# Performance work log

Measured on AMD Instinct MI355X. Metric: run time of the kernel, lower is better.

Reference implementation:

```python
import jax, jax.numpy as jnp
import numpy as np

B, N, D, H, DK = 4, 2048, 1024, 16, 64  # batch, seq, model_dim, heads, key_dim (= value_dim)
NEG = -1e9


def setup_inputs() -> dict:
    key = jax.random.key(0)
    ks = jax.random.split(key, 5)
    X = jax.random.normal(ks[0], (B, N, D), dtype=jnp.float32)
    # causal additive mask [N, N]; module slices mask[:N, :M] and adds to logits
    mask = jnp.where(jnp.tril(jnp.ones((N, N), dtype=bool)), 0.0, NEG).astype(jnp.float32)
    s = 1.0 / np.sqrt(D)
    Wq = jax.random.normal(ks[1], (D, H * DK), dtype=jnp.float32) * s
    Wk = jax.random.normal(ks[2], (D, H * DK), dtype=jnp.float32) * s
    Wv = jax.random.normal(ks[3], (D, H * DK), dtype=jnp.float32) * s
    Wo = jax.random.normal(ks[4], (H * DK, D), dtype=jnp.float32) * s
    return {"X": X, "mask": mask, "Wq": Wq, "Wk": Wk, "Wv": Wv, "Wo": Wo}


def reference(X, mask, Wq, Wk, Wv, Wo):
    # Linear projections (bias=False), then split heads: [B,N,H,DK] -> [B,H,N,DK]
    Q = (X @ Wq).reshape(B, N, H, DK).transpose(0, 2, 1, 3)
    K = (X @ Wk).reshape(B, N, H, DK).transpose(0, 2, 1, 3)
    V = (X @ Wv).reshape(B, N, H, DK).transpose(0, 2, 1, 3)
    # full [B,H,N,N] attention logits (module materializes it explicitly)
    att = jnp.einsum('bhnd,bhmd->bhnm', Q, K) / jnp.sqrt(jnp.float32(DK))
    # dropout is in eval mode here -> identity; then additive mask[:N,:M]
    att = att + mask[:N, :N]
    prob = jax.nn.softmax(att, axis=-1)
    values = jnp.einsum('bhnm,bhmd->bhnd', prob, V)
    values_cat = values.transpose(0, 2, 1, 3).reshape(B, N, H * DK)
    return values_cat @ Wo
```

## Files before the change

kernel.cpp:

```cpp
#include <hip/hip_runtime.h>

typedef __fp16   f2  __attribute__((ext_vector_type(2)));
typedef _Float16 h4  __attribute__((ext_vector_type(4)));
typedef _Float16 v8h __attribute__((ext_vector_type(8)));
typedef float    v4f __attribute__((ext_vector_type(4)));
struct f2x2 { f2 lo, hi; };

constexpr int Bn = 4, Nn = 2048, Dn = 1024, Hn = 16, DKn = 64, Mn = 8192;

__device__ __forceinline__ void load_lds16(const _Float16* g, _Float16* l) {
    __builtin_amdgcn_global_load_lds(
        (const __attribute__((address_space(1))) void*)g,
        (__attribute__((address_space(3))) void*)l, 16, 0, 0);
}

__global__ __launch_bounds__(256) void cast_f16(const float* __restrict__ x,
                                                _Float16* __restrict__ y) {
    const int i = blockIdx.x * 256 + threadIdx.x;
    const float4 v = ((const float4*)x)[i];
    h4 o; o[0] = (_Float16)v.x; o[1] = (_Float16)v.y;
    o[2] = (_Float16)v.z; o[3] = (_Float16)v.w;
    ((h4*)y)[i] = o;
}

__global__ __launch_bounds__(256) void castW4(const float* __restrict__ Wq,
                                              const float* __restrict__ Wk,
                                              const float* __restrict__ Wv,
                                              const float* __restrict__ Wo,
                                              _Float16* __restrict__ Wqkv,
                                              _Float16* __restrict__ Wto) {
    __shared__ float tile[32][33];
    const int which = blockIdx.x >> 10, bid = blockIdx.x & 1023;
    const float* W = which == 0 ? Wq : which == 1 ? Wk : which == 2 ? Wv : Wo;
    _Float16* Dst = which < 3 ? (Wqkv + ((size_t)which << 20)) : Wto;
    const int bx = bid & 31, by = bid >> 5;
    const int t = threadIdx.x;
    const int r = t >> 3, c4 = (t & 7) * 4;
    const float4 v = *(const float4*)&W[(size_t)(by * 32 + r) * Dn + bx * 32 + c4];
    tile[r][c4 + 0] = v.x; tile[r][c4 + 1] = v.y;
    tile[r][c4 + 2] = v.z; tile[r][c4 + 3] = v.w;
    __syncthreads();
    h4 o;
    o[0] = (_Float16)tile[c4 + 0][r];
    o[1] = (_Float16)tile[c4 + 1][r];
    o[2] = (_Float16)tile[c4 + 2][r];
    o[3] = (_Float16)tile[c4 + 3][r];
    *(h4*)&Dst[(size_t)(bx * 32 + r) * Dn + by * 32 + c4] = o;
}

#define GEMM_KLOOP64(Abase, Bbase)                                                  \
    v4f acc[4][4];                                                                  \
    _Pragma("unroll") for (int i = 0; i < 4; ++i)                                   \
        _Pragma("unroll") for (int j = 0; j < 4; ++j) acc[i][j] = v4f{0,0,0,0};     \
    for (int k0 = 0; k0 < Dn; k0 += 64) {                                           \
        __syncthreads();                                                            \
        _Pragma("unroll") for (int jj = 0; jj < 4; ++jj) {                          \
            const int ci = jj * 256 + w * 64 + lane;                                \
            const int rs = ci >> 3, cs = ci & 7;                                    \
            const int gc = (cs ^ (rs & 7)) * 8;                                     \
            load_lds16(Abase + (size_t)rs * Dn + k0 + gc, &As[(jj*256 + w*64) * 8]);\
            load_lds16(Bbase + (size_t)rs * Dn + k0 + gc, &Bs[(jj*256 + w*64) * 8]);\
        }                                                                           \
        __syncthreads();                                                            \
        _Pragma("unroll") for (int ks2 = 0; ks2 < 2; ++ks2) {                       \
            v8h a[4], b[4];                                                         \
            _Pragma("unroll") for (int i = 0; i < 4; ++i) {                         \
                const int ar = wm*64 + i*16 + l16;                                  \
                a[i] = *(const v8h*)&As[ar * 64 + (((ks2*4 + quad) ^ (ar & 7)) * 8)];\
            }                                                                       \
            _Pragma("unroll") for (int j = 0; j < 4; ++j) {                         \
                const int br = wn*64 + j*16 + l16;                                  \
                b[j] = *(const v8h*)&Bs[br * 64 + (((ks2*4 + quad) ^ (br & 7)) * 8)];\
            }                                                                       \
            _Pragma("unroll") for (int i = 0; i < 4; ++i)                           \
                _Pragma("unroll") for (int j = 0; j < 4; ++j)                       \
                    acc[i][j] = __builtin_amdgcn_mfma_f32_16x16x32_f16(a[i], b[j],  \
                                                                   acc[i][j],0,0,0);\
        }                                                                           \
    }

__global__ __launch_bounds__(256) void gemmqkv(const _Float16* __restrict__ A,
                                               const _Float16* __restrict__ Wt,
                                               _Float16* __restrict__ Qo,
                                               _Float16* __restrict__ Ko,
                                               _Float16* __restrict__ Vo)
{
    __shared__ __align__(16) _Float16 As[128 * 64];
    __shared__ __align__(16) _Float16 Bs[128 * 64];
    const int t = threadIdx.x, lane = t & 63, w = t >> 6;
    const int quad = lane >> 4, l16 = lane & 15;
    const int wm = w >> 1, wn = w & 1;
    const int bx = blockIdx.x % 24, by = blockIdx.x / 24;
    const int m0 = by * 128, n0 = bx * 128;
    const _Float16* Abase = A + (size_t)m0 * Dn;
    const _Float16* Bbase = Wt + (size_t)n0 * Dn;

    GEMM_KLOOP64(Abase, Bbase)

    const int sec = n0 >> 10;
    if (sec < 2) {
        _Float16* C = sec ? Ko : Qo;
        const float scale = sec ? 1.0f : 0.125f * 1.44269504f;
#pragma unroll
        for (int i = 0; i < 4; ++i) {
            const int mbase = m0 + wm * 64 + i * 16 + quad * 4;
#pragma unroll
            for (int j = 0; j < 4; ++j) {
                const int nl = (n0 + wn * 64 + j * 16 + l16) & 1023;
                const int h = nl >> 6, dk = nl & 63;
#pragma unroll
                for (int r = 0; r < 4; ++r) {
                    const int m = mbase + r, b = m >> 11, nr = m & (Nn - 1);
                    C[((size_t)(b * Hn + h) * Nn + nr) * DKn + dk] = (_Float16)(acc[i][j][r] * scale);
                }
            }
        }
    } else {
#pragma unroll
        for (int i = 0; i < 4; ++i) {
            const int mbase = m0 + wm * 64 + i * 16 + quad * 4;
            const int b = mbase >> 11, nr = mbase & (Nn - 1);
#pragma unroll
            for (int j = 0; j < 4; ++j) {
                const int nl = (n0 + wn * 64 + j * 16 + l16) & 1023;
                const int h = nl >> 6, dk = nl & 63;
                h4 o; o[0] = (_Float16)acc[i][j][0]; o[1] = (_Float16)acc[i][j][1];
                o[2] = (_Float16)acc[i][j][2]; o[3] = (_Float16)acc[i][j][3];
                *(h4*)&Vo[((size_t)(b * Hn + h) * DKn + dk) * Nn + nr] = o;
            }
        }
    }
}

__global__ __launch_bounds__(256) void gemmo(const _Float16* __restrict__ A,
                                             const _Float16* __restrict__ Wt,
                                             float* __restrict__ C)
{
    __shared__ __align__(16) _Float16 As[128 * 64];
    __shared__ __align__(16) _Float16 Bs[128 * 64];
    const int t = threadIdx.x, lane = t & 63, w = t >> 6;
    const int quad = lane >> 4, l16 = lane & 15;
    const int wm = w >> 1, wn = w & 1;
    const int bx = blockIdx.x & 7, by = blockIdx.x >> 3;
    const int m0 = by * 128, n0 = bx * 128;
    const _Float16* Abase = A + (size_t)m0 * Dn;
    const _Float16* Bbase = Wt + (size_t)n0 * Dn;

    GEMM_KLOOP64(Abase, Bbase)

#pragma unroll
    for (int i = 0; i < 4; ++i) {
        const int mbase = m0 + wm * 64 + i * 16 + quad * 4;
#pragma unroll
        for (int j = 0; j < 4; ++j) {
            const int n = n0 + wn * 64 + j * 16 + l16;
#pragma unroll
            for (int r = 0; r < 4; ++r)
                C[(size_t)(mbase + r) * Dn + n] = acc[i][j][r];
        }
    }
}

__global__ __launch_bounds__(256) void flashv5(const _Float16* __restrict__ Q,
                                               const _Float16* __restrict__ K,
                                               const _Float16* __restrict__ Vt,
                                               _Float16* __restrict__ O)
{
    __shared__ __align__(16) _Float16 KS[64 * 64];
    __shared__ __align__(16) _Float16 VS[64 * 64];
    __shared__ __align__(16) _Float16 Ps[4][32 * 64];

    const int t = threadIdx.x;
    const int lane = t & 63, w = t >> 6;
    const int quad = lane >> 4, l16 = lane & 15;
    const int bh = blockIdx.x & 63;
    const int qtile = 15 - (blockIdx.x >> 6);
    const int b = bh >> 4, h = bh & 15;
    const int qb = qtile * 128 + w * 32;

    const _Float16* Qg = Q  + (size_t)bh * Nn * DKn;
    const _Float16* Kg = K  + (size_t)bh * Nn * DKn;
    const _Float16* Vg = Vt + (size_t)bh * DKn * Nn;

    auto stage = [&](int kt) {
        const int k0 = kt * 64;
#pragma unroll
        for (int jj = 0; jj < 2; ++jj) {
            const int ci = jj * 256 + w * 64 + lane;
            const int r = ci >> 3, c = ci & 7;
            const int gc = (c ^ (r & 7)) * 8;
            load_lds16(Kg + (size_t)(k0 + r) * DKn + gc, &KS[(jj * 256 + w * 64) * 8]);
            load_lds16(Vg + (size_t)r * Nn + k0 + gc,    &VS[(jj * 256 + w * 64) * 8]);
        }
    };
#define SWZ(arr, r, c) (*(const v8h*)&(arr)[(r) * 64 + (((c) ^ ((r) & 7)) * 8)])

    v8h qf[2][2];
#pragma unroll
    for (int qq = 0; qq < 2; ++qq)
#pragma unroll
        for (int ks = 0; ks < 2; ++ks)
            qf[qq][ks] = *(const v8h*)&Qg[(size_t)(qb + qq * 16 + l16) * DKn + ks * 32 + quad * 8];

    v8h ones;
#pragma unroll
    for (int i = 0; i < 8; ++i) ones[i] = (_Float16)1.0f;

    v4f o[2][4];
#pragma unroll
    for (int mq = 0; mq < 2; ++mq)
#pragma unroll
        for (int nt = 0; nt < 4; ++nt) o[mq][nt] = v4f{0.f, 0.f, 0.f, 0.f};
    v4f ol[2] = {v4f{0.f, 0.f, 0.f, 0.f}, v4f{0.f, 0.f, 0.f, 0.f}};

    const int NKT  = 2 * qtile + 2;
    const int diag = 2 * qtile + (w >> 1);

    for (int kt = 0; kt < NKT; ++kt) {
        stage(kt);
        __syncthreads();
        if (kt <= diag) {
            const int k0 = kt * 64;
            auto ptile = [&](bool domask) {
#pragma unroll
                for (int kk = 0; kk < 4; ++kk) {
                    v4f s0 = v4f{0.f, 0.f, 0.f, 0.f}, s1 = v4f{0.f, 0.f, 0.f, 0.f};
#pragma unroll
                    for (int ks = 0; ks < 2; ++ks) {
                        const v8h ak = SWZ(KS, kk * 16 + l16, ks * 4 + quad);
                        s0 = __builtin_amdgcn_mfma_f32_16x16x32_f16(ak, qf[0][ks], s0, 0, 0, 0);
                        s1 = __builtin_amdgcn_mfma_f32_16x16x32_f16(ak, qf[1][ks], s1, 0, 0, 0);
                    }
                    const int key0 = k0 + kk * 16 + quad * 4;
#pragma unroll
                    for (int qq = 0; qq < 2; ++qq) {
                        const v4f sv = qq ? s1 : s0;
                        const int q = qb + qq * 16 + l16;
                        float p[4];
#pragma unroll
                        for (int r = 0; r < 4; ++r) {
                            float x = sv[r];
                            if (domask) x = (key0 + r > q) ? -1e9f : x;
                            p[r] = exp2f(x);
                        }
                        f2x2 pkr;
                        pkr.lo = __builtin_amdgcn_cvt_pkrtz(p[0], p[1]);
                        pkr.hi = __builtin_amdgcn_cvt_pkrtz(p[2], p[3]);
                        const h4 pk = __builtin_bit_cast(h4, pkr);
                        const int prow = qq * 16 + l16;
                        const int pch  = kk * 2 + (quad >> 1);
                        *(h4*)&Ps[w][prow * 64 + ((pch ^ (prow & 7)) * 8 + (quad & 1) * 4)] = pk;
                    }
                }
#pragma unroll
                for (int ks = 0; ks < 2; ++ks)
#pragma unroll
                    for (int mq = 0; mq < 2; ++mq) {
                        const int arow = mq * 16 + l16;
                        const int ach  = ks * 4 + quad;
                        const v8h a = *(const v8h*)&Ps[w][arow * 64 + ((ach ^ (arow & 7)) * 8)];
#pragma unroll
                        for (int nt = 0; nt < 4; ++nt) {
                            const v8h bvv = SWZ(VS, nt * 16 + l16, ks * 4 + quad);
                            o[mq][nt] = __builtin_amdgcn_mfma_f32_16x16x32_f16(a, bvv, o[mq][nt], 0, 0, 0);
                        }
                        ol[mq] = __builtin_amdgcn_mfma_f32_16x16x32_f16(a, ones, ol[mq], 0, 0, 0);
                    }
            };
            if (kt == diag) ptile(true); else ptile(false);
        }
        __syncthreads();
    }
#undef SWZ

    _Float16* Op = O + (size_t)b * Nn * Dn + h * DKn;
#pragma unroll
    for (int mq = 0; mq < 2; ++mq)
#pragma unroll
        for (int r = 0; r < 4; ++r) {
            const float li = 1.0f / ol[mq][r];
            const int qrow = qb + mq * 16 + quad * 4 + r;
#pragma unroll
            for (int nt = 0; nt < 4; ++nt)
                Op[(size_t)qrow * Dn + nt * 16 + l16] = (_Float16)(o[mq][nt][r] * li);
        }
}

extern "C" void kernel_launch(void* const* d_in, const int* in_sizes, int n_in,
                              void* d_out, int out_size, void* d_ws, size_t ws_size,
                              hipStream_t stream)
{
    const float* X  = (const float*)d_in[0];
    const float* Wq = (const float*)d_in[2];
    const float* Wk = (const float*)d_in[3];
    const float* Wv = (const float*)d_in[4];
    const float* Wo = (const float*)d_in[5];

    char* ws = (char*)d_ws;
    _Float16* Xh   = (_Float16*)ws;
    _Float16* Wqkv = (_Float16*)(ws + (16u << 20));
    _Float16* Wto  = Wqkv + (3u << 20);
    _Float16* Qh   = Wto + (1u << 20);
    _Float16* Kh   = Qh + (size_t)Mn * Dn;
    _Float16* Vth  = Kh + (size_t)Mn * Dn;
    _Float16* Ah   = Vth + (size_t)Mn * Dn;

    cast_f16<<<(Mn * Dn / 4) / 256, 256, 0, stream>>>(X, Xh);
    castW4<<<4096, 256, 0, stream>>>(Wq, Wk, Wv, Wo, Wqkv, Wto);
    gemmqkv<<<64 * 24, 256, 0, stream>>>(Xh, Wqkv, Qh, Kh, Vth);
    flashv5<<<1024, 256, 0, stream>>>(Qh, Kh, Vth, Ah);
    gemmo<<<512, 256, 0, stream>>>(Ah, Wto, (float*)d_out);
}
```

Measured before the change: 262.6 us.

## Shrink output GEMM tile to 128x64, precompute LDS offsets, use native exp2

The output projection GEMM now uses 128x64 tiles with its own inline K-loop, doubling the grid to 1024 blocks so more CUs have work. In the flash attention kernel, swizzled LDS offsets for K, V and P are computed once per thread instead of inside the loop, and exp2f is replaced by the hardware exp2 builtin when it is available. The trade-offs are more redundant A-tile loads in the GEMM, extra registers held for the offset tables in attention, and possibly slightly different exp2 accuracy.

```diff
diff --git a/kernel.cpp b/kernel.cpp
--- a/kernel.cpp
+++ b/kernel.cpp
@@ -5,6 +5,12 @@
 typedef _Float16 v8h __attribute__((ext_vector_type(8)));
 typedef float    v4f __attribute__((ext_vector_type(4)));
 struct f2x2 { f2 lo, hi; };
+
+#if __has_builtin(__builtin_amdgcn_exp2f)
+#define FEXP2(x) __builtin_amdgcn_exp2f(x)
+#else
+#define FEXP2(x) exp2f(x)
+#endif
 
 constexpr int Bn = 4, Nn = 2048, Dn = 1024, Hn = 16, DKn = 64, Mn = 8192;
 
@@ -137,23 +143,65 @@
                                              float* __restrict__ C)
 {
     __shared__ __align__(16) _Float16 As[128 * 64];
-    __shared__ __align__(16) _Float16 Bs[128 * 64];
+    __shared__ __align__(16) _Float16 Bs[64 * 64];
     const int t = threadIdx.x, lane = t & 63, w = t >> 6;
     const int quad = lane >> 4, l16 = lane & 15;
     const int wm = w >> 1, wn = w & 1;
-    const int bx = blockIdx.x & 7, by = blockIdx.x >> 3;
-    const int m0 = by * 128, n0 = bx * 128;
+    const int bx = blockIdx.x & 15, by = blockIdx.x >> 4;
+    const int m0 = by * 128, n0 = bx * 64;
     const _Float16* Abase = A + (size_t)m0 * Dn;
     const _Float16* Bbase = Wt + (size_t)n0 * Dn;
 
-    GEMM_KLOOP64(Abase, Bbase)
+    v4f acc[4][2];
+#pragma unroll
+    for (int i = 0; i < 4; ++i)
+#pragma unroll
+        for (int j = 0; j < 2; ++j) acc[i][j] = v4f{0.f, 0.f, 0.f, 0.f};
+
+    for (int k0 = 0; k0 < Dn; k0 += 64) {
+        __syncthreads();
+#pragma unroll
+        for (int jj = 0; jj < 4; ++jj) {
+            const int ci = jj * 256 + w * 64 + lane;
+            const int rs = ci >> 3, cs = ci & 7;
+            const int gc = (cs ^ (rs & 7)) * 8;
+            load_lds16(Abase + (size_t)rs * Dn + k0 + gc, &As[(jj * 256 + w * 64) * 8]);
+        }
+#pragma unroll
+        for (int jj = 0; jj < 2; ++jj) {
+            const int ci = jj * 256 + w * 64 + lane;
+            const int rs = ci >> 3, cs = ci & 7;
+            const int gc = (cs ^ (rs & 7)) * 8;
+            load_lds16(Bbase + (size_t)rs * Dn + k0 + gc, &Bs[(jj * 256 + w * 64) * 8]);
+        }
+        __syncthreads();
+#pragma unroll
+        for (int ks2 = 0; ks2 < 2; ++ks2) {
+            v8h a[4], b[2];
+#pragma unroll
+            for (int i = 0; i < 4; ++i) {
+                const int ar = wm * 64 + i * 16 + l16;
+                a[i] = *(const v8h*)&As[ar * 64 + (((ks2 * 4 + quad) ^ (ar & 7)) * 8)];
+            }
+#pragma unroll
+            for (int j = 0; j < 2; ++j) {
+                const int br = wn * 32 + j * 16 + l16;
+                b[j] = *(const v8h*)&Bs[br * 64 + (((ks2 * 4 + quad) ^ (br & 7)) * 8)];
+            }
+#pragma unroll
+            for (int i = 0; i < 4; ++i)
+#pragma unroll
+                for (int j = 0; j < 2; ++j)
+                    acc[i][j] = __builtin_amdgcn_mfma_f32_16x16x32_f16(a[i], b[j], acc[i][j], 0, 0, 0);
+        }
+    }
 
 #pragma unroll
     for (int i = 0; i < 4; ++i) {
         const int mbase = m0 + wm * 64 + i * 16 + quad * 4;
 #pragma unroll
-        for (int j = 0; j < 4; ++j) {
-            const int n = n0 + wn * 64 + j * 16 + l16;
+        for (int j = 0; j < 2; ++j) {
+            const int n = n0 + wn * 32 + j * 16 + l16;
 #pragma unroll
             for (int r = 0; r < 4; ++r)
                 C[(size_t)(mbase + r) * Dn + n] = acc[i][j][r];
@@ -193,7 +241,6 @@
             load_lds16(Vg + (size_t)r * Nn + k0 + gc,    &VS[(jj * 256 + w * 64) * 8]);
         }
     };
-#define SWZ(arr, r, c) (*(const v8h*)&(arr)[(r) * 64 + (((c) ^ ((r) & 7)) * 8)])
 
     v8h qf[2][2];
 #pragma unroll
@@ -201,6 +248,31 @@
 #pragma unroll
         for (int ks = 0; ks < 2; ++ks)
             qf[qq][ks] = *(const v8h*)&Qg[(size_t)(qb + qq * 16 + l16) * DKn + ks * 32 + quad * 8];
+
+    int koff[4][2], voff[4][2], pwoff[2][4], proff[2][2];
+#pragma unroll
+    for (int kk = 0; kk < 4; ++kk)
+#pragma unroll
+        for (int ks = 0; ks < 2; ++ks) {
+            const int kr = kk * 16 + l16, kc = ks * 4 + quad;
+            koff[kk][ks] = kr * 64 + ((kc ^ (kr & 7)) * 8);
+            const int vr = kk * 16 + l16;
+            voff[kk][ks] = vr * 64 + ((kc ^ (vr & 7)) * 8);
+        }
+#pragma unroll
+    for (int qq = 0; qq < 2; ++qq) {
+        const int prow = qq * 16 + l16;
+#pragma unroll
+        for (int kk = 0; kk < 4; ++kk) {
+            const int pch = kk * 2 + (quad >> 1);
+            pwoff[qq][kk] = prow * 64 + ((pch ^ (prow & 7)) * 8 + (quad & 1) * 4);
+        }
+#pragma unroll
+        for (int ks = 0; ks < 2; ++ks) {
+            const int ach = ks * 4 + quad;
+            proff[qq][ks] = prow * 64 + ((ach ^ (prow & 7)) * 8);
+        }
+    }
 
     v8h ones;
 #pragma unroll
@@ -227,7 +299,7 @@
                     v4f s0 = v4f{0.f, 0.f, 0.f, 0.f}, s1 = v4f{0.f, 0.f, 0.f, 0.f};
 #pragma unroll
                     for (int ks = 0; ks < 2; ++ks) {
-                        const v8h ak = SWZ(KS, kk * 16 + l16, ks * 4 + quad);
+                        const v8h ak = *(const v8h*)&KS[koff[kk][ks]];
                         s0 = __builtin_amdgcn_mfma_f32_16x16x32_f16(ak, qf[0][ks], s0, 0, 0, 0);
                         s1 = __builtin_amdgcn_mfma_f32_16x16x32_f16(ak, qf[1][ks], s1, 0, 0, 0);
                     }
@@ -241,27 +313,23 @@
                         for (int r = 0; r < 4; ++r) {
                             float x = sv[r];
                             if (domask) x = (key0 + r > q) ? -1e9f : x;
-                            p[r] = exp2f(x);
+                            p[r] = FEXP2(x);
                         }
                         f2x2 pkr;
                         pkr.lo = __builtin_amdgcn_cvt_pkrtz(p[0], p[1]);
                         pkr.hi = __builtin_amdgcn_cvt_pkrtz(p[2], p[3]);
                         const h4 pk = __builtin_bit_cast(h4, pkr);
-                        const int prow = qq * 16 + l16;
-                        const int pch  = kk * 2 + (quad >> 1);
-                        *(h4*)&Ps[w][prow * 64 + ((pch ^ (prow & 7)) * 8 + (quad & 1) * 4)] = pk;
+                        *(h4*)&Ps[w][pwoff[qq][kk]] = pk;
                     }
                 }
 #pragma unroll
                 for (int ks = 0; ks < 2; ++ks)
 #pragma unroll
                     for (int mq = 0; mq < 2; ++mq) {
-                        const int arow = mq * 16 + l16;
-                        const int ach  = ks * 4 + quad;
-                        const v8h a = *(const v8h*)&Ps[w][arow * 64 + ((ach ^ (arow & 7)) * 8)];
+                        const v8h a = *(const v8h*)&Ps[w][proff[mq][ks]];
 #pragma unroll
                         for (int nt = 0; nt < 4; ++nt) {
-                            const v8h bvv = SWZ(VS, nt * 16 + l16, ks * 4 + quad);
+                            const v8h bvv = *(const v8h*)&VS[voff[nt][ks]];
                             o[mq][nt] = __builtin_amdgcn_mfma_f32_16x16x32_f16(a, bvv, o[mq][nt], 0, 0, 0);
                         }
                         ol[mq] = __builtin_amdgcn_mfma_f32_16x16x32_f16(a, ones, ol[mq], 0, 0, 0);
@@ -271,7 +339,6 @@
         }
         __syncthreads();
     }
-#undef SWZ
 
     _Float16* Op = O + (size_t)b * Nn * Dn + h * DKn;
 #pragma unroll
@@ -309,5 +376,5 @@
     castW4<<<4096, 256, 0, stream>>>(Wq, Wk, Wv, Wo, Wqkv, Wto);
     gemmqkv<<<64 * 24, 256, 0, stream>>>(Xh, Wqkv, Qh, Kh, Vth);
     flashv5<<<1024, 256, 0, stream>>>(Qh, Kh, Vth, Ah);
-    gemmo<<<512, 256, 0, stream>>>(Ah, Wto, (float*)d_out);
-}
+    gemmo<<<1024, 256, 0, stream>>>(Ah, Wto, (float*)d_out);
+}
```

After: 275.9 us. 1.05x slower.
